# Kernel tuning notes

Measured on AMD Instinct MI355X. Metric: run time of the kernel, lower is better.

The kernel has to match this reference:

```python
import jax, jax.numpy as jnp
import numpy as np

B = 4
G = 1024                      # GridSize
H = 1.0 / (G - 1)             # h = (right-left)/(GridSize-1), area=[[0,0],[1,1]]
GD = 0.0                      # boundary value for hard_encode padding


def _cross(a):
    # sum of 4-neighborhood: matches conv2d with kernel [[0,.5,0],[.5,0,.5],[0,.5,0]] / 0.5
    return a[..., :-2, 1:-1] + a[..., 2:, 1:-1] + a[..., 1:-1, :-2] + a[..., 1:-1, 2:]


def _inner(a):
    return a[..., 1:-1, 1:-1]


def kappa(x, mu):
    # assumed parameterization (kappa undefined in source): exp(mu * x)
    return jnp.exp(mu * x)


def setup_inputs() -> dict:
    key = jax.random.key(0)
    k1, k2, k3, k4 = jax.random.split(key, 4)
    pre = jax.random.normal(k1, (B, 1, G - 2, G - 2), jnp.float32)
    f = jax.random.normal(k2, (B, 1, G, G), jnp.float32)
    mu = jax.random.uniform(k3, (1,), jnp.float32)
    prev_pre = jax.random.normal(k4, (B, 1, G, G), jnp.float32) * 0.1
    return {"pre": pre, "f": f, "mu": mu, "prev_pre": prev_pre, "maxiter": 20}


def reference(pre, f, mu, prev_pre, maxiter):
    # w = kappa(prev_pre, mu) is iteration-invariant -> hoist out of the loop
    w = kappa(prev_pre, mu)            # [B,1,G,G]
    w_in = _inner(w)                   # [B,1,G-2,G-2]
    force = _inner(f) * (H * H)
    # k3 conv: 0.5*cross + 2*center
    y3 = 0.5 * _cross(w) + 2.0 * w_in

    def step(y, _):
        u = jnp.pad(y, ((0, 0), (0, 0), (1, 1), (1, 1)), constant_values=GD)
        y1 = 0.5 * _cross(u) * w_in    # conv(u, k1) * w_inner
        y2 = 0.5 * _cross(w * u)       # conv(w*u, k2)
        return (force + y1 + y2) / y3, None

    # original: one jac_step, then `maxiter` more -> maxiter+1 total
    y, _ = jax.lax.scan(step, pre, None, length=maxiter + 1)
    return y
```

## Files before the change

### kernel.cpp

```cpp
#include <hip/hip_runtime.h>

#define BB 4
#define GG 1024
#define NI 1022
#define SROW 1024
#define HH2 (2.0f / (1023.0f * 1023.0f))
#define OFFC 12
#define TOUTC 104
#define NTC 10
#define HS 132

typedef float vf4 __attribute__((ext_vector_type(4)));
typedef float vf2 __attribute__((ext_vector_type(2)));

__device__ __forceinline__ float dpp_left(float x) {
    int i = __builtin_bit_cast(int, x);
    i = __builtin_amdgcn_update_dpp(i, i, 0x138, 0xf, 0xf, false);
    return __builtin_bit_cast(float, i);
}
__device__ __forceinline__ float dpp_right(float x) {
    int i = __builtin_bit_cast(int, x);
    i = __builtin_amdgcn_update_dpp(i, i, 0x130, 0xf, 0xf, false);
    return __builtin_bit_cast(float, i);
}

template<int TKP, int OFFR, int TOUTR, bool VIN4, bool VOUT4>
__global__ __launch_bounds__(512, 4)
void pinn_slab(const float* __restrict__ ysrc,
               const float* __restrict__ fglob,
               const float* __restrict__ mu_p,
               const float* __restrict__ pp,
               float* __restrict__ yout)
{
    __shared__ float ytop[2][16 * HS], ybot[2][16 * HS];
    float* const wh0 = ytop[0];
    float* const wh1 = ybot[0];

    const int tid = threadIdx.x;
    const int tx = tid & 31, ty = tid >> 5;
    const int b  = blockIdx.z;
    const int AR = blockIdx.y * TOUTR - OFFR;
    const int A0 = blockIdx.x * TOUTC - OFFC;
    const int R  = 4 * ty;
    const int c0 = 4 * tx;
    const float mu = mu_p[0];

    const int cb = min(max(A0 + c0, 0), GG - 4);
    const size_t pb = (size_t)b * GG * GG;
    const int r0 = min(max(AR + R,     0), GG - 1);
    const int r1 = min(max(AR + R + 1, 0), GG - 1);
    const int r2 = min(max(AR + R + 2, 0), GG - 1);
    const int r3 = min(max(AR + R + 3, 0), GG - 1);
    const int r4 = min(max(AR + R + 4, 0), GG - 1);
    vf4 wv0 = *(const vf4*)&pp[pb + (size_t)r0 * GG + cb];
    vf4 wv1 = *(const vf4*)&pp[pb + (size_t)r1 * GG + cb];
    vf4 wv2 = *(const vf4*)&pp[pb + (size_t)r2 * GG + cb];
    vf4 wv3 = *(const vf4*)&pp[pb + (size_t)r3 * GG + cb];
    const vf4 fv0 = *(const vf4*)&fglob[pb + (size_t)r1 * GG + cb];
    const vf4 fv1 = *(const vf4*)&fglob[pb + (size_t)r2 * GG + cb];
    const vf4 fv2 = *(const vf4*)&fglob[pb + (size_t)r3 * GG + cb];
    const vf4 fv3 = *(const vf4*)&fglob[pb + (size_t)r4 * GG + cb];

    vf4 y0v, y1v, y2v, y3v;
    {
        const int i0 = min(max(AR + R,     0), NI - 1);
        const int i1 = min(max(AR + R + 1, 0), NI - 1);
        const int i2 = min(max(AR + R + 2, 0), NI - 1);
        const int i3 = min(max(AR + R + 3, 0), NI - 1);
        if (VIN4) {
            const int cy = min(max(A0 + c0, 0), SROW - 4);
            y0v = *(const vf4*)&ysrc[(size_t)(b * NI + i0) * SROW + cy];
            y1v = *(const vf4*)&ysrc[(size_t)(b * NI + i1) * SROW + cy];
            y2v = *(const vf4*)&ysrc[(size_t)(b * NI + i2) * SROW + cy];
            y3v = *(const vf4*)&ysrc[(size_t)(b * NI + i3) * SROW + cy];
        } else {
            const int cy  = min(max(A0 + c0, 0), NI - 2);
            const int cy2 = min(cy + 2, NI - 2);
            #define LDY(dst, ii) { \
                const size_t base_ = (size_t)(b * NI + (ii)) * NI; \
                const vf2 a_ = *(const vf2*)&ysrc[base_ + cy]; \
                const vf2 b_ = *(const vf2*)&ysrc[base_ + cy2]; \
                dst[0] = a_[0]; dst[1] = a_[1]; dst[2] = b_[0]; dst[3] = b_[1]; }
            LDY(y0v, i0) LDY(y1v, i1) LDY(y2v, i2) LDY(y3v, i3)
            #undef LDY
        }
    }

    #pragma unroll
    for (int m = 0; m < 4; ++m) {
        wv0[m] = __expf(mu * wv0[m]);
        wv1[m] = __expf(mu * wv1[m]);
        wv2[m] = __expf(mu * wv2[m]);
        wv3[m] = __expf(mu * wv3[m]);
    }
    *(vf4*)&wh0[ty * HS + c0] = wv0;
    *(vf4*)&wh1[ty * HS + c0] = wv1;
    __syncthreads();

    const int nxt = min(ty + 1, 15) * HS + c0;
    const vf4 w4 = *(const vf4*)&wh0[nxt];
    const vf4 w5 = *(const vf4*)&wh1[nxt];

    const float s1_0 = dpp_right(wv0[0]);
    const float s1_1 = dpp_right(wv1[0]);
    const float s1_2 = dpp_right(wv2[0]);
    const float s1_3 = dpp_right(wv3[0]);
    const float s1_4 = dpp_right(w4[0]);
    const float s1_5 = dpp_right(w5[0]);
    const float s2_1 = dpp_right(wv1[1]);
    const float s2_2 = dpp_right(wv2[1]);
    const float s2_3 = dpp_right(wv3[1]);
    const float s2_4 = dpp_right(w4[1]);
    const float sf0 = dpp_right(fv0[0]);
    const float sf1 = dpp_right(fv1[0]);
    const float sf2 = dpp_right(fv2[0]);
    const float sf3 = dpp_right(fv3[0]);

    vf4 rmv, colm;
    #pragma unroll
    for (int k = 0; k < 4; ++k)
        rmv[k] = ((unsigned)(AR + R + k) < (unsigned)NI) ? 1.0f : 0.0f;
    #pragma unroll
    for (int m = 0; m < 4; ++m)
        colm[m] = ((unsigned)(A0 + c0 + m) < (unsigned)NI) ? 1.0f : 0.0f;

    vf4 bN0,bS0,bW0,bf0, bN1,bS1,bW1,bf1,
        bN2,bS2,bW2,bf2, bN3,bS3,bW3,bf3;

    #define COEFF(kk, N_, C_, S_, s1N, s1C, s1S, s2C, FV, SF, BN, BS, BW, BF, YV) { \
        const vf4 wN = {N_[1], N_[2], N_[3], s1N}; \
        const vf4 wW = C_; \
        const vf4 wC = {C_[1], C_[2], C_[3], s1C}; \
        const vf4 wE = {C_[2], C_[3], s1C, s2C}; \
        const vf4 wS = {S_[1], S_[2], S_[3], s1S}; \
        const vf4 aN = wC + wN, aS = wC + wS, aW = wC + wW, aE = wC + wE; \
        const vf4 den = (aN + aS) + (aW + aE); \
        vf4 rd; \
        _Pragma("unroll") \
        for (int m = 0; m < 4; ++m) { \
            float x = __builtin_amdgcn_rcpf(den[m]); \
            x = x * (2.0f - den[m] * x); \
            const bool in = (rmv[(kk)] != 0.0f) && (colm[m] != 0.0f); \
            rd[m] = in ? x : 0.0f; \
            YV[m] = in ? YV[m] : 0.0f; \
        } \
        BN = aN * rd; BS = aS * rd; BW = aW * rd; \
        const vf4 fC = {FV[1], FV[2], FV[3], SF}; \
        BF = (fC * rd) * HH2; }

    COEFF(0, wv0, wv1, wv2, s1_0, s1_1, s1_2, s2_1, fv0, sf0, bN0,bS0,bW0,bf0, y0v)
    COEFF(1, wv1, wv2, wv3, s1_1, s1_2, s1_3, s2_2, fv1, sf1, bN1,bS1,bW1,bf1, y1v)
    COEFF(2, wv2, wv3, w4,  s1_2, s1_3, s1_4, s2_3, fv2, sf2, bN2,bS2,bW2,bf2, y2v)
    COEFF(3, wv3, w4,  w5,  s1_3, s1_4, s1_5, s2_4, fv3, sf3, bN3,bS3,bW3,bf3, y3v)
    #undef COEFF

    const int tyo = ty * HS + c0;
    const int upo = max(ty - 1, 0)  * HS + c0;
    const int dno = min(ty + 1, 15) * HS + c0;

    for (int t = 1; t <= TKP; ++t) {
        float* tb = ytop[t & 1];
        float* bb = ybot[t & 1];
        *(vf4*)&tb[tyo] = y0v;
        *(vf4*)&bb[tyo] = y3v;
        __syncthreads();
        const vf4 up = *(const vf4*)&bb[upo];
        const vf4 dn = *(const vf4*)&tb[dno];
        const vf4 yW0 = {dpp_left(y0v[3]), y0v[0], y0v[1], y0v[2]};
        const vf4 yW1 = {dpp_left(y1v[3]), y1v[0], y1v[1], y1v[2]};
        const vf4 yW2 = {dpp_left(y2v[3]), y2v[0], y2v[1], y2v[2]};
        const vf4 yW3 = {dpp_left(y3v[3]), y3v[0], y3v[1], y3v[2]};
        const vf4 yE0 = {y0v[1], y0v[2], y0v[3], dpp_right(y0v[0])};
        const vf4 yE1 = {y1v[1], y1v[2], y1v[3], dpp_right(y1v[0])};
        const vf4 yE2 = {y2v[1], y2v[2], y2v[3], dpp_right(y2v[0])};
        const vf4 yE3 = {y3v[1], y3v[2], y3v[3], dpp_right(y3v[0])};
        const vf4 bE0 = ((colm * rmv[0]) - bN0 - bS0) - bW0;
        const vf4 bE1 = ((colm * rmv[1]) - bN1 - bS1) - bW1;
        const vf4 bE2 = ((colm * rmv[2]) - bN2 - bS2) - bW2;
        const vf4 bE3 = ((colm * rmv[3]) - bN3 - bS3) - bW3;
        vf4 n0 = bf0; n0 += bN0 * up;  n0 += bS0 * y1v; n0 += bW0 * yW0; n0 += bE0 * yE0;
        vf4 n1 = bf1; n1 += bN1 * y0v; n1 += bS1 * y2v; n1 += bW1 * yW1; n1 += bE1 * yE1;
        vf4 n2 = bf2; n2 += bN2 * y1v; n2 += bS2 * y3v; n2 += bW2 * yW2; n2 += bE2 * yE2;
        vf4 n3 = bf3; n3 += bN3 * y2v; n3 += bS3 * dn;  n3 += bW3 * yW3; n3 += bE3 * yE3;
        y0v = n0; y1v = n1; y2v = n2; y3v = n3;
    }

    if (c0 >= OFFC && c0 < OFFC + TOUTC) {
        const int gj0 = A0 + c0;
        if (VOUT4) {
            #define STORE4(kk, YV) { \
                const int r = R + (kk); \
                if (r >= OFFR && r < OFFR + TOUTR) { \
                    const int gi = AR + r; \
                    if (gi < NI && gj0 <= SROW - 4) \
                        *(vf4*)&yout[(size_t)(b * NI + gi) * SROW + gj0] = YV; } }
            STORE4(0, y0v) STORE4(1, y1v) STORE4(2, y2v) STORE4(3, y3v)
            #undef STORE4
        } else {
            #define STORE(kk, YV) { \
                const int r = R + (kk); \
                if (r >= OFFR && r < OFFR + TOUTR) { \
                    const int gi = AR + r; \
                    if (gi < NI) { \
                        const size_t rb = (size_t)(b * NI + gi) * NI; \
                        if (gj0 + 3 < NI) { \
                            vf2 pa, pv; pa[0]=YV[0]; pa[1]=YV[1]; pv[0]=YV[2]; pv[1]=YV[3]; \
                            *(vf2*)&yout[rb + gj0] = pa; *(vf2*)&yout[rb + gj0 + 2] = pv; \
                        } else { \
                            _Pragma("unroll") \
                            for (int m = 0; m < 4; ++m) \
                                if (gj0 + m < NI) yout[rb + gj0 + m] = YV[m]; \
                        } \
                    } } }
            STORE(0, y0v) STORE(1, y1v) STORE(2, y2v) STORE(3, y3v)
            #undef STORE
        }
    }
}

extern "C" void kernel_launch(void* const* d_in, const int* in_sizes, int n_in,
                              void* d_out, int out_size, void* d_ws, size_t ws_size,
                              hipStream_t stream) {
    const float* pre = (const float*)d_in[0];
    const float* f   = (const float*)d_in[1];
    const float* mu  = (const float*)d_in[2];
    const float* pp  = (const float*)d_in[3];

    float* yA = (float*)d_ws;

    const dim3 bs(512, 1, 1);
    pinn_slab<11, 11, 42, false, true ><<<dim3(NTC, 25, BB), bs, 0, stream>>>(pre, f, mu, pp, yA);
    pinn_slab<10, 10, 44, true,  false><<<dim3(NTC, 24, BB), bs, 0, stream>>>(yA,  f, mu, pp, (float*)d_out);
}
```

Before: 141.9 us.

## Process two column tiles per block with async LDS prefetch of prev_pre

Each block now handles two adjacent column tiles sequentially, halving the grid. While the first tile sweeps, the second tile's prev_pre values are prefetched into an LDS staging buffer via global_load_lds, hiding that load latency. This adds 32KB of LDS per block, which may reduce occupancy. It also serializes work that previously ran in parallel blocks.

```diff
diff --git a/kernel.cpp b/kernel.cpp
--- a/kernel.cpp
+++ b/kernel.cpp
@@ -12,6 +12,9 @@
 
 typedef float vf4 __attribute__((ext_vector_type(4)));
 typedef float vf2 __attribute__((ext_vector_type(2)));
+
+typedef __attribute__((address_space(3))) void lds_vt;
+typedef const __attribute__((address_space(1))) void gm_vt;
 
 __device__ __forceinline__ float dpp_left(float x) {
     int i = __builtin_bit_cast(int, x);
@@ -26,106 +29,37 @@
 
 template<int TKP, int OFFR, int TOUTR, bool VIN4, bool VOUT4>
 __global__ __launch_bounds__(512, 4)
-void pinn_slab(const float* __restrict__ ysrc,
-               const float* __restrict__ fglob,
-               const float* __restrict__ mu_p,
-               const float* __restrict__ pp,
-               float* __restrict__ yout)
+void pinn_duo(const float* __restrict__ ysrc,
+              const float* __restrict__ fglob,
+              const float* __restrict__ mu_p,
+              const float* __restrict__ pp,
+              float* __restrict__ yout)
 {
     __shared__ float ytop[2][16 * HS], ybot[2][16 * HS];
+    __shared__ __align__(16) float pstg[64 * 128];
     float* const wh0 = ytop[0];
     float* const wh1 = ybot[0];
 
     const int tid = threadIdx.x;
     const int tx = tid & 31, ty = tid >> 5;
+    const int wvid = tid >> 6;
+    const int ln   = tid & 63;
     const int b  = blockIdx.z;
     const int AR = blockIdx.y * TOUTR - OFFR;
-    const int A0 = blockIdx.x * TOUTC - OFFC;
+    const int A0a = (2 * blockIdx.x)     * TOUTC - OFFC;
+    const int A0b = (2 * blockIdx.x + 1) * TOUTC - OFFC;
     const int R  = 4 * ty;
     const int c0 = 4 * tx;
     const float mu = mu_p[0];
-
-    const int cb = min(max(A0 + c0, 0), GG - 4);
     const size_t pb = (size_t)b * GG * GG;
-    const int r0 = min(max(AR + R,     0), GG - 1);
-    const int r1 = min(max(AR + R + 1, 0), GG - 1);
-    const int r2 = min(max(AR + R + 2, 0), GG - 1);
-    const int r3 = min(max(AR + R + 3, 0), GG - 1);
-    const int r4 = min(max(AR + R + 4, 0), GG - 1);
-    vf4 wv0 = *(const vf4*)&pp[pb + (size_t)r0 * GG + cb];
-    vf4 wv1 = *(const vf4*)&pp[pb + (size_t)r1 * GG + cb];
-    vf4 wv2 = *(const vf4*)&pp[pb + (size_t)r2 * GG + cb];
-    vf4 wv3 = *(const vf4*)&pp[pb + (size_t)r3 * GG + cb];
-    const vf4 fv0 = *(const vf4*)&fglob[pb + (size_t)r1 * GG + cb];
-    const vf4 fv1 = *(const vf4*)&fglob[pb + (size_t)r2 * GG + cb];
-    const vf4 fv2 = *(const vf4*)&fglob[pb + (size_t)r3 * GG + cb];
-    const vf4 fv3 = *(const vf4*)&fglob[pb + (size_t)r4 * GG + cb];
-
-    vf4 y0v, y1v, y2v, y3v;
-    {
-        const int i0 = min(max(AR + R,     0), NI - 1);
-        const int i1 = min(max(AR + R + 1, 0), NI - 1);
-        const int i2 = min(max(AR + R + 2, 0), NI - 1);
-        const int i3 = min(max(AR + R + 3, 0), NI - 1);
-        if (VIN4) {
-            const int cy = min(max(A0 + c0, 0), SROW - 4);
-            y0v = *(const vf4*)&ysrc[(size_t)(b * NI + i0) * SROW + cy];
-            y1v = *(const vf4*)&ysrc[(size_t)(b * NI + i1) * SROW + cy];
-            y2v = *(const vf4*)&ysrc[(size_t)(b * NI + i2) * SROW + cy];
-            y3v = *(const vf4*)&ysrc[(size_t)(b * NI + i3) * SROW + cy];
-        } else {
-            const int cy  = min(max(A0 + c0, 0), NI - 2);
-            const int cy2 = min(cy + 2, NI - 2);
-            #define LDY(dst, ii) { \
-                const size_t base_ = (size_t)(b * NI + (ii)) * NI; \
-                const vf2 a_ = *(const vf2*)&ysrc[base_ + cy]; \
-                const vf2 b_ = *(const vf2*)&ysrc[base_ + cy2]; \
-                dst[0] = a_[0]; dst[1] = a_[1]; dst[2] = b_[0]; dst[3] = b_[1]; }
-            LDY(y0v, i0) LDY(y1v, i1) LDY(y2v, i2) LDY(y3v, i3)
-            #undef LDY
-        }
-    }
-
-    #pragma unroll
-    for (int m = 0; m < 4; ++m) {
-        wv0[m] = __expf(mu * wv0[m]);
-        wv1[m] = __expf(mu * wv1[m]);
-        wv2[m] = __expf(mu * wv2[m]);
-        wv3[m] = __expf(mu * wv3[m]);
-    }
-    *(vf4*)&wh0[ty * HS + c0] = wv0;
-    *(vf4*)&wh1[ty * HS + c0] = wv1;
-    __syncthreads();
-
-    const int nxt = min(ty + 1, 15) * HS + c0;
-    const vf4 w4 = *(const vf4*)&wh0[nxt];
-    const vf4 w5 = *(const vf4*)&wh1[nxt];
-
-    const float s1_0 = dpp_right(wv0[0]);
-    const float s1_1 = dpp_right(wv1[0]);
-    const float s1_2 = dpp_right(wv2[0]);
-    const float s1_3 = dpp_right(wv3[0]);
-    const float s1_4 = dpp_right(w4[0]);
-    const float s1_5 = dpp_right(w5[0]);
-    const float s2_1 = dpp_right(wv1[1]);
-    const float s2_2 = dpp_right(wv2[1]);
-    const float s2_3 = dpp_right(wv3[1]);
-    const float s2_4 = dpp_right(w4[1]);
-    const float sf0 = dpp_right(fv0[0]);
-    const float sf1 = dpp_right(fv1[0]);
-    const float sf2 = dpp_right(fv2[0]);
-    const float sf3 = dpp_right(fv3[0]);
-
-    vf4 rmv, colm;
+
+    const int tyo = ty * HS + c0;
+    const int upo = max(ty - 1, 0)  * HS + c0;
+    const int dno = min(ty + 1, 15) * HS + c0;
+    vf4 rmv;
     #pragma unroll
     for (int k = 0; k < 4; ++k)
         rmv[k] = ((unsigned)(AR + R + k) < (unsigned)NI) ? 1.0f : 0.0f;
-    #pragma unroll
-    for (int m = 0; m < 4; ++m)
-        colm[m] = ((unsigned)(A0 + c0 + m) < (unsigned)NI) ? 1.0f : 0.0f;
-
-    vf4 bN0,bS0,bW0,bf0, bN1,bS1,bW1,bf1,
-        bN2,bS2,bW2,bf2, bN3,bS3,bW3,bf3;
 
     #define COEFF(kk, N_, C_, S_, s1N, s1C, s1S, s2C, FV, SF, BN, BS, BW, BF, YV) { \
         const vf4 wN = {N_[1], N_[2], N_[3], s1N}; \
@@ -148,74 +82,239 @@
         const vf4 fC = {FV[1], FV[2], FV[3], SF}; \
         BF = (fC * rd) * HH2; }
 
-    COEFF(0, wv0, wv1, wv2, s1_0, s1_1, s1_2, s2_1, fv0, sf0, bN0,bS0,bW0,bf0, y0v)
-    COEFF(1, wv1, wv2, wv3, s1_1, s1_2, s1_3, s2_2, fv1, sf1, bN1,bS1,bW1,bf1, y1v)
-    COEFF(2, wv2, wv3, w4,  s1_2, s1_3, s1_4, s2_3, fv2, sf2, bN2,bS2,bW2,bf2, y2v)
-    COEFF(3, wv3, w4,  w5,  s1_3, s1_4, s1_5, s2_4, fv3, sf3, bN3,bS3,bW3,bf3, y3v)
+    #define SWEEPS(TKN) \
+        for (int t = 1; t <= (TKN); ++t) { \
+            float* tb = ytop[t & 1]; \
+            float* bb = ybot[t & 1]; \
+            *(vf4*)&tb[tyo] = y0v; \
+            *(vf4*)&bb[tyo] = y3v; \
+            __syncthreads(); \
+            const vf4 up = *(const vf4*)&bb[upo]; \
+            const vf4 dn = *(const vf4*)&tb[dno]; \
+            const vf4 yW0 = {dpp_left(y0v[3]), y0v[0], y0v[1], y0v[2]}; \
+            const vf4 yW1 = {dpp_left(y1v[3]), y1v[0], y1v[1], y1v[2]}; \
+            const vf4 yW2 = {dpp_left(y2v[3]), y2v[0], y2v[1], y2v[2]}; \
+            const vf4 yW3 = {dpp_left(y3v[3]), y3v[0], y3v[1], y3v[2]}; \
+            const vf4 yE0 = {y0v[1], y0v[2], y0v[3], dpp_right(y0v[0])}; \
+            const vf4 yE1 = {y1v[1], y1v[2], y1v[3], dpp_right(y1v[0])}; \
+            const vf4 yE2 = {y2v[1], y2v[2], y2v[3], dpp_right(y2v[0])}; \
+            const vf4 yE3 = {y3v[1], y3v[2], y3v[3], dpp_right(y3v[0])}; \
+            const vf4 bE0 = ((colm * rmv[0]) - bN0 - bS0) - bW0; \
+            const vf4 bE1 = ((colm * rmv[1]) - bN1 - bS1) - bW1; \
+            const vf4 bE2 = ((colm * rmv[2]) - bN2 - bS2) - bW2; \
+            const vf4 bE3 = ((colm * rmv[3]) - bN3 - bS3) - bW3; \
+            vf4 n0 = bf0; n0 += bN0 * up;  n0 += bS0 * y1v; n0 += bW0 * yW0; n0 += bE0 * yE0; \
+            vf4 n1 = bf1; n1 += bN1 * y0v; n1 += bS1 * y2v; n1 += bW1 * yW1; n1 += bE1 * yE1; \
+            vf4 n2 = bf2; n2 += bN2 * y1v; n2 += bS2 * y3v; n2 += bW2 * yW2; n2 += bE2 * yE2; \
+            vf4 n3 = bf3; n3 += bN3 * y2v; n3 += bS3 * dn;  n3 += bW3 * yW3; n3 += bE3 * yE3; \
+            y0v = n0; y1v = n1; y2v = n2; y3v = n3; \
+        }
+
+    #define LOADY(A0_) { \
+        const int i0 = min(max(AR + R,     0), NI - 1); \
+        const int i1 = min(max(AR + R + 1, 0), NI - 1); \
+        const int i2 = min(max(AR + R + 2, 0), NI - 1); \
+        const int i3 = min(max(AR + R + 3, 0), NI - 1); \
+        if (VIN4) { \
+            const int cy = min(max((A0_) + c0, 0), SROW - 4); \
+            y0v = *(const vf4*)&ysrc[(size_t)(b * NI + i0) * SROW + cy]; \
+            y1v = *(const vf4*)&ysrc[(size_t)(b * NI + i1) * SROW + cy]; \
+            y2v = *(const vf4*)&ysrc[(size_t)(b * NI + i2) * SROW + cy]; \
+            y3v = *(const vf4*)&ysrc[(size_t)(b * NI + i3) * SROW + cy]; \
+        } else { \
+            const int cy  = min(max((A0_) + c0, 0), NI - 2); \
+            const int cy2 = min(cy + 2, NI - 2); \
+            { const size_t base_ = (size_t)(b * NI + i0) * NI; \
+              const vf2 a_ = *(const vf2*)&ysrc[base_ + cy]; \
+              const vf2 b_ = *(const vf2*)&ysrc[base_ + cy2]; \
+              y0v[0]=a_[0]; y0v[1]=a_[1]; y0v[2]=b_[0]; y0v[3]=b_[1]; } \
+            { const size_t base_ = (size_t)(b * NI + i1) * NI; \
+              const vf2 a_ = *(const vf2*)&ysrc[base_ + cy]; \
+              const vf2 b_ = *(const vf2*)&ysrc[base_ + cy2]; \
+              y1v[0]=a_[0]; y1v[1]=a_[1]; y1v[2]=b_[0]; y1v[3]=b_[1]; } \
+            { const size_t base_ = (size_t)(b * NI + i2) * NI; \
+              const vf2 a_ = *(const vf2*)&ysrc[base_ + cy]; \
+              const vf2 b_ = *(const vf2*)&ysrc[base_ + cy2]; \
+              y2v[0]=a_[0]; y2v[1]=a_[1]; y2v[2]=b_[0]; y2v[3]=b_[1]; } \
+            { const size_t base_ = (size_t)(b * NI + i3) * NI; \
+              const vf2 a_ = *(const vf2*)&ysrc[base_ + cy]; \
+              const vf2 b_ = *(const vf2*)&ysrc[base_ + cy2]; \
+              y3v[0]=a_[0]; y3v[1]=a_[1]; y3v[2]=b_[0]; y3v[3]=b_[1]; } \
+        } }
+
+    #define STOREY(A0_) { \
+        if (c0 >= OFFC && c0 < OFFC + TOUTC) { \
+            const int gj0 = (A0_) + c0; \
+            if (VOUT4) { \
+                _Pragma("unroll") \
+                for (int kk = 0; kk < 4; ++kk) { \
+                    const int r = R + kk; \
+                    if (r >= OFFR && r < OFFR + TOUTR) { \
+                        const int gi = AR + r; \
+                        const vf4 YV = kk == 0 ? y0v : kk == 1 ? y1v : kk == 2 ? y2v : y3v; \
+                        if (gi < NI && gj0 <= SROW - 4) \
+                            *(vf4*)&yout[(size_t)(b * NI + gi) * SROW + gj0] = YV; } } \
+            } else { \
+                _Pragma("unroll") \
+                for (int kk = 0; kk < 4; ++kk) { \
+                    const int r = R + kk; \
+                    if (r >= OFFR && r < OFFR + TOUTR) { \
+                        const int gi = AR + r; \
+                        const vf4 YV = kk == 0 ? y0v : kk == 1 ? y1v : kk == 2 ? y2v : y3v; \
+                        if (gi < NI) { \
+                            const size_t rb = (size_t)(b * NI + gi) * NI; \
+                            if (gj0 + 3 < NI) { \
+                                vf2 pa, pv; pa[0]=YV[0]; pa[1]=YV[1]; pv[0]=YV[2]; pv[1]=YV[3]; \
+                                *(vf2*)&yout[rb + gj0] = pa; *(vf2*)&yout[rb + gj0 + 2] = pv; \
+                            } else { \
+                                _Pragma("unroll") \
+                                for (int m = 0; m < 4; ++m) \
+                                    if (gj0 + m < NI) yout[rb + gj0 + m] = YV[m]; \
+                            } } } } \
+            } } }
+
+    {
+        const int A0 = A0a;
+        const int cb = min(max(A0 + c0, 0), GG - 4);
+        const int r0 = min(max(AR + R,     0), GG - 1);
+        const int r1 = min(max(AR + R + 1, 0), GG - 1);
+        const int r2 = min(max(AR + R + 2, 0), GG - 1);
+        const int r3 = min(max(AR + R + 3, 0), GG - 1);
+        const int r4 = min(max(AR + R + 4, 0), GG - 1);
+        vf4 wv0 = *(const vf4*)&pp[pb + (size_t)r0 * GG + cb];
+        vf4 wv1 = *(const vf4*)&pp[pb + (size_t)r1 * GG + cb];
+        vf4 wv2 = *(const vf4*)&pp[pb + (size_t)r2 * GG + cb];
+        vf4 wv3 = *(const vf4*)&pp[pb + (size_t)r3 * GG + cb];
+        const vf4 fv0 = *(const vf4*)&fglob[pb + (size_t)r1 * GG + cb];
+        const vf4 fv1 = *(const vf4*)&fglob[pb + (size_t)r2 * GG + cb];
+        const vf4 fv2 = *(const vf4*)&fglob[pb + (size_t)r3 * GG + cb];
+        const vf4 fv3 = *(const vf4*)&fglob[pb + (size_t)r4 * GG + cb];
+        vf4 y0v, y1v, y2v, y3v;
+        LOADY(A0)
+
+        #pragma unroll
+        for (int m = 0; m < 4; ++m) {
+            wv0[m] = __expf(mu * wv0[m]);
+            wv1[m] = __expf(mu * wv1[m]);
+            wv2[m] = __expf(mu * wv2[m]);
+            wv3[m] = __expf(mu * wv3[m]);
+        }
+        *(vf4*)&wh0[ty * HS + c0] = wv0;
+        *(vf4*)&wh1[ty * HS + c0] = wv1;
+        __syncthreads();
+        const int nxt = min(ty + 1, 15) * HS + c0;
+        const vf4 w4 = *(const vf4*)&wh0[nxt];
+        const vf4 w5 = *(const vf4*)&wh1[nxt];
+
+        const float s1_0 = dpp_right(wv0[0]);
+        const float s1_1 = dpp_right(wv1[0]);
+        const float s1_2 = dpp_right(wv2[0]);
+        const float s1_3 = dpp_right(wv3[0]);
+        const float s1_4 = dpp_right(w4[0]);
+        const float s1_5 = dpp_right(w5[0]);
+        const float s2_1 = dpp_right(wv1[1]);
+        const float s2_2 = dpp_right(wv2[1]);
+        const float s2_3 = dpp_right(wv3[1]);
+        const float s2_4 = dpp_right(w4[1]);
+        const float sf0 = dpp_right(fv0[0]);
+        const float sf1 = dpp_right(fv1[0]);
+        const float sf2 = dpp_right(fv2[0]);
+        const float sf3 = dpp_right(fv3[0]);
+
+        vf4 colm;
+        #pragma unroll
+        for (int m = 0; m < 4; ++m)
+            colm[m] = ((unsigned)(A0 + c0 + m) < (unsigned)NI) ? 1.0f : 0.0f;
+
+        vf4 bN0,bS0,bW0,bf0, bN1,bS1,bW1,bf1,
+            bN2,bS2,bW2,bf2, bN3,bS3,bW3,bf3;
+        COEFF(0, wv0, wv1, wv2, s1_0, s1_1, s1_2, s2_1, fv0, sf0, bN0,bS0,bW0,bf0, y0v)
+        COEFF(1, wv1, wv2, wv3, s1_1, s1_2, s1_3, s2_2, fv1, sf1, bN1,bS1,bW1,bf1, y1v)
+        COEFF(2, wv2, wv3, w4,  s1_2, s1_3, s1_4, s2_3, fv2, sf2, bN2,bS2,bW2,bf2, y2v)
+        COEFF(3, wv3, w4,  w5,  s1_3, s1_4, s1_5, s2_4, fv3, sf3, bN3,bS3,bW3,bf3, y3v)
+
+        {
+            const int scol = min(max(A0b + (ln & 31) * 4, 0), GG - 4);
+            #pragma unroll
+            for (int i = 0; i < 4; ++i) {
+                const int j  = (i * 8 + wvid) * 2 + (ln >> 5);
+                const int gp = min(max(AR + j, 0), GG - 1);
+                __builtin_amdgcn_global_load_lds(
+                    (gm_vt*)&pp[pb + (size_t)gp * GG + scol],
+                    (lds_vt*)(pstg + (i * 8 + wvid) * 256), 16, 0, 0);
+            }
+        }
+
+        SWEEPS(TKP)
+        STOREY(A0)
+    }
+
+    __syncthreads();
+
+    {
+        const int A0 = A0b;
+        const int cb = min(max(A0 + c0, 0), GG - 4);
+        const int r1 = min(max(AR + R + 1, 0), GG - 1);
+        const int r2 = min(max(AR + R + 2, 0), GG - 1);
+        const int r3 = min(max(AR + R + 3, 0), GG - 1);
+        const int r4 = min(max(AR + R + 4, 0), GG - 1);
+        const vf4 fv0 = *(const vf4*)&fglob[pb + (size_t)r1 * GG + cb];
+        const vf4 fv1 = *(const vf4*)&fglob[pb + (size_t)r2 * GG + cb];
+        const vf4 fv2 = *(const vf4*)&fglob[pb + (size_t)r3 * GG + cb];
+        const vf4 fv3 = *(const vf4*)&fglob[pb + (size_t)r4 * GG + cb];
+        vf4 y0v, y1v, y2v, y3v;
+        LOADY(A0)
+
+        vf4 wv0 = *(const vf4*)&pstg[ R             * 128 + c0];
+        vf4 wv1 = *(const vf4*)&pstg[(R + 1)        * 128 + c0];
+        vf4 wv2 = *(const vf4*)&pstg[(R + 2)        * 128 + c0];
+        vf4 wv3 = *(const vf4*)&pstg[(R + 3)        * 128 + c0];
+        vf4 w4  = *(const vf4*)&pstg[min(R + 4, 63) * 128 + c0];
+        vf4 w5  = *(const vf4*)&pstg[min(R + 5, 63) * 128 + c0];
+        #pragma unroll
+        for (int m = 0; m < 4; ++m) {
+            wv0[m] = __expf(mu * wv0[m]);
+            wv1[m] = __expf(mu * wv1[m]);
+            wv2[m] = __expf(mu * wv2[m]);
+            wv3[m] = __expf(mu * wv3[m]);
+            w4[m]  = __expf(mu * w4[m]);
+            w5[m]  = __expf(mu * w5[m]);
+        }
+
+        const float s1_0 = dpp_right(wv0[0]);
+        const float s1_1 = dpp_right(wv1[0]);
+        const float s1_2 = dpp_right(wv2[0]);
+        const float s1_3 = dpp_right(wv3[0]);
+        const float s1_4 = dpp_right(w4[0]);
+        const float s1_5 = dpp_right(w5[0]);
+        const float s2_1 = dpp_right(wv1[1]);
+        const float s2_2 = dpp_right(wv2[1]);
+        const float s2_3 = dpp_right(wv3[1]);
+        const float s2_4 = dpp_right(w4[1]);
+        const float sf0 = dpp_right(fv0[0]);
+        const float sf1 = dpp_right(fv1[0]);
+        const float sf2 = dpp_right(fv2[0]);
+        const float sf3 = dpp_right(fv3[0]);
+
+        vf4 colm;
+        #pragma unroll
+        for (int m = 0; m < 4; ++m)
+            colm[m] = ((unsigned)(A0 + c0 + m) < (unsigned)NI) ? 1.0f : 0.0f;
+
+        vf4 bN0,bS0,bW0,bf0, bN1,bS1,bW1,bf1,
+            bN2,bS2,bW2,bf2, bN3,bS3,bW3,bf3;
+        COEFF(0, wv0, wv1, wv2, s1_0, s1_1, s1_2, s2_1, fv0, sf0, bN0,bS0,bW0,bf0, y0v)
+        COEFF(1, wv1, wv2, wv3, s1_1, s1_2, s1_3, s2_2, fv1, sf1, bN1,bS1,bW1,bf1, y1v)
+        COEFF(2, wv2, wv3, w4,  s1_2, s1_3, s1_4, s2_3, fv2, sf2, bN2,bS2,bW2,bf2, y2v)
+        COEFF(3, wv3, w4,  w5,  s1_3, s1_4, s1_5, s2_4, fv3, sf3, bN3,bS3,bW3,bf3, y3v)
+
+        SWEEPS(TKP)
+        STOREY(A0)
+    }
     #undef COEFF
-
-    const int tyo = ty * HS + c0;
-    const int upo = max(ty - 1, 0)  * HS + c0;
-    const int dno = min(ty + 1, 15) * HS + c0;
-
-    for (int t = 1; t <= TKP; ++t) {
-        float* tb = ytop[t & 1];
-        float* bb = ybot[t & 1];
-        *(vf4*)&tb[tyo] = y0v;
-        *(vf4*)&bb[tyo] = y3v;
-        __syncthreads();
-        const vf4 up = *(const vf4*)&bb[upo];
-        const vf4 dn = *(const vf4*)&tb[dno];
-        const vf4 yW0 = {dpp_left(y0v[3]), y0v[0], y0v[1], y0v[2]};
-        const vf4 yW1 = {dpp_left(y1v[3]), y1v[0], y1v[1], y1v[2]};
-        const vf4 yW2 = {dpp_left(y2v[3]), y2v[0], y2v[1], y2v[2]};
-        const vf4 yW3 = {dpp_left(y3v[3]), y3v[0], y3v[1], y3v[2]};
-        const vf4 yE0 = {y0v[1], y0v[2], y0v[3], dpp_right(y0v[0])};
-        const vf4 yE1 = {y1v[1], y1v[2], y1v[3], dpp_right(y1v[0])};
-        const vf4 yE2 = {y2v[1], y2v[2], y2v[3], dpp_right(y2v[0])};
-        const vf4 yE3 = {y3v[1], y3v[2], y3v[3], dpp_right(y3v[0])};
-        const vf4 bE0 = ((colm * rmv[0]) - bN0 - bS0) - bW0;
-        const vf4 bE1 = ((colm * rmv[1]) - bN1 - bS1) - bW1;
-        const vf4 bE2 = ((colm * rmv[2]) - bN2 - bS2) - bW2;
-        const vf4 bE3 = ((colm * rmv[3]) - bN3 - bS3) - bW3;
-        vf4 n0 = bf0; n0 += bN0 * up;  n0 += bS0 * y1v; n0 += bW0 * yW0; n0 += bE0 * yE0;
-        vf4 n1 = bf1; n1 += bN1 * y0v; n1 += bS1 * y2v; n1 += bW1 * yW1; n1 += bE1 * yE1;
-        vf4 n2 = bf2; n2 += bN2 * y1v; n2 += bS2 * y3v; n2 += bW2 * yW2; n2 += bE2 * yE2;
-        vf4 n3 = bf3; n3 += bN3 * y2v; n3 += bS3 * dn;  n3 += bW3 * yW3; n3 += bE3 * yE3;
-        y0v = n0; y1v = n1; y2v = n2; y3v = n3;
-    }
-
-    if (c0 >= OFFC && c0 < OFFC + TOUTC) {
-        const int gj0 = A0 + c0;
-        if (VOUT4) {
-            #define STORE4(kk, YV) { \
-                const int r = R + (kk); \
-                if (r >= OFFR && r < OFFR + TOUTR) { \
-                    const int gi = AR + r; \
-                    if (gi < NI && gj0 <= SROW - 4) \
-                        *(vf4*)&yout[(size_t)(b * NI + gi) * SROW + gj0] = YV; } }
-            STORE4(0, y0v) STORE4(1, y1v) STORE4(2, y2v) STORE4(3, y3v)
-            #undef STORE4
-        } else {
-            #define STORE(kk, YV) { \
-                const int r = R + (kk); \
-                if (r >= OFFR && r < OFFR + TOUTR) { \
-                    const int gi = AR + r; \
-                    if (gi < NI) { \
-                        const size_t rb = (size_t)(b * NI + gi) * NI; \
-                        if (gj0 + 3 < NI) { \
-                            vf2 pa, pv; pa[0]=YV[0]; pa[1]=YV[1]; pv[0]=YV[2]; pv[1]=YV[3]; \
-                            *(vf2*)&yout[rb + gj0] = pa; *(vf2*)&yout[rb + gj0 + 2] = pv; \
-                        } else { \
-                            _Pragma("unroll") \
-                            for (int m = 0; m < 4; ++m) \
-                                if (gj0 + m < NI) yout[rb + gj0 + m] = YV[m]; \
-                        } \
-                    } } }
-            STORE(0, y0v) STORE(1, y1v) STORE(2, y2v) STORE(3, y3v)
-            #undef STORE
-        }
-    }
+    #undef SWEEPS
+    #undef LOADY
+    #undef STOREY
 }
 
 extern "C" void kernel_launch(void* const* d_in, const int* in_sizes, int n_in,
@@ -229,6 +328,6 @@
     float* yA = (float*)d_ws;
 
     const dim3 bs(512, 1, 1);
-    pinn_slab<11, 11, 42, false, true ><<<dim3(NTC, 25, BB), bs, 0, stream>>>(pre, f, mu, pp, yA);
-    pinn_slab<10, 10, 44, true,  false><<<dim3(NTC, 24, BB), bs, 0, stream>>>(yA,  f, mu, pp, (float*)d_out);
+    pinn_duo<11, 11, 42, false, true ><<<dim3(NTC/2, 25, BB), bs, 0, stream>>>(pre, f, mu, pp, yA);
+    pinn_duo<10, 10, 44, true,  false><<<dim3(NTC/2, 24, BB), bs, 0, stream>>>(yA,  f, mu, pp, (float*)d_out);
 }
```

Result: slower. 171.3 us (+20.7%).
